# Performance work log

Measured on AMD Instinct MI355X. Metric: run time of the kernel, lower is better.

Reference implementation:

```python
import jax, jax.numpy as jnp
import numpy as np

B, S, E, H = 2, 2048, 1024, 16
D = E // H  # head_dim = 64


def setup_inputs() -> dict:
    key = jax.random.key(0)
    ks = jax.random.split(key, 6)
    scale = 1.0 / np.sqrt(E)
    x = jax.random.normal(ks[0], (B, S, E), dtype=jnp.float32)
    mask = jnp.ones((B, S), dtype=jnp.int32)
    Wqkv = jax.random.normal(ks[1], (E, 3 * E), dtype=jnp.float32) * scale
    bqkv = jax.random.normal(ks[2], (3 * E,), dtype=jnp.float32) * 0.01
    Wout = jax.random.normal(ks[3], (E, E), dtype=jnp.float32) * scale
    bout = jax.random.normal(ks[4], (E,), dtype=jnp.float32) * 0.01
    return {"x": x, "mask": mask, "Wqkv": Wqkv, "bqkv": bqkv, "Wout": Wout, "bout": bout}


def reference(x, mask, Wqkv, bqkv, Wout, bout):
    Bn, Sn, En = x.shape
    qkv = x @ Wqkv + bqkv                      # [B,S,3E]
    qkv = qkv.reshape(Bn, Sn, 3, H, D)
    qkv = jnp.transpose(qkv, (2, 0, 3, 1, 4))  # [3,B,H,S,D]
    q, k, v = qkv[0], qkv[1], qkv[2]
    scores = jnp.einsum('bhqd,bhkd->bhqk', q, k) / np.sqrt(D).astype(np.float32)
    m = mask[:, None, None, :]                 # [B,1,1,S]
    scores = jnp.where(m == 0, jnp.float32(-jnp.inf), scores)
    attn = jax.nn.softmax(scores, axis=-1)
    out = jnp.einsum('bhqk,bhkd->bhqd', attn, v)  # [B,H,S,D]
    out = jnp.transpose(out, (0, 2, 1, 3)).reshape(Bn, Sn, En)
    return out @ Wout + bout
```

## Files before the change

### kernel.cpp

```cpp
#include <hip/hip_runtime.h>


typedef __attribute__((ext_vector_type(8))) short short8;
typedef __attribute__((ext_vector_type(4))) short short4b;
typedef __attribute__((ext_vector_type(4))) float floatx4;
typedef unsigned short ushort_t;

static __device__ __forceinline__ ushort_t f2bf(float f) {
    unsigned u = __float_as_uint(f);
    u += 0x7fffu + ((u >> 16) & 1u);
    return (ushort_t)(u >> 16);
}
static __device__ __forceinline__ float bf2f(ushort_t h) {
    return __uint_as_float(((unsigned)h) << 16);
}
#if __has_builtin(__builtin_amdgcn_cvt_pk_bf16_f32)
typedef __attribute__((ext_vector_type(2))) __bf16 bf16x2_t;
static __device__ __forceinline__ unsigned pack2bf(float a, float b) {
    bf16x2_t r = __builtin_amdgcn_cvt_pk_bf16_f32(a, b);
    return __builtin_bit_cast(unsigned, r);
}
#else
static __device__ __forceinline__ unsigned pack2bf(float a, float b) {
    return (unsigned)f2bf(a) | ((unsigned)f2bf(b) << 16);
}
#endif
static __device__ __forceinline__ float hexp2(float x) {
    return __builtin_amdgcn_exp2f(x);
}
static __device__ __forceinline__ void gload16(const void* g, void* l) {
    __builtin_amdgcn_global_load_lds(
        (const __attribute__((address_space(1))) unsigned int*)g,
        (__attribute__((address_space(3))) unsigned int*)l, 16, 0, 0);
}

static __device__ __forceinline__ floatx4 mfma16(short4b a, short4b b, floatx4 c) {
#if __has_builtin(__builtin_amdgcn_mfma_f32_16x16x16_bf16)
    return __builtin_amdgcn_mfma_f32_16x16x16_bf16(a, b, c, 0, 0, 0);
#elif __has_builtin(__builtin_amdgcn_mfma_f32_16x16x16bf16_1k)
    return __builtin_amdgcn_mfma_f32_16x16x16bf16_1k(a, b, c, 0, 0, 0);
#else
    asm("v_mfma_f32_16x16x16_bf16 %0, %1, %2, %0" : "+v"(c) : "v"(a), "v"(b));
    return c;
#endif
}

__global__ __launch_bounds__(256) void prep(
    const float* __restrict__ x, ushort_t* __restrict__ xb,
    const float* __restrict__ Wqkv, ushort_t* __restrict__ wqT,
    const float* __restrict__ Wout, ushort_t* __restrict__ woT,
    const int* __restrict__ mask, float* __restrict__ maddg)
{
    __shared__ float tile[32][33];
    const int bk = blockIdx.x;
    const int t = threadIdx.x;
    if (bk < 4096) {
        int i = bk * 256 + t;
        float4 v = ((const float4*)x)[i];
        uint2 o;
        o.x = pack2bf(v.x, v.y);
        o.y = pack2bf(v.z, v.w);
        ((uint2*)xb)[i] = o;
        return;
    }
    if (bk < 8192) {
        const float* W; ushort_t* WT; int K, N, id;
        if (bk < 7168) { W = Wqkv; WT = wqT; K = 1024; N = 3072; id = bk - 4096;
                         int nb = (id % 96) * 32, kb = (id / 96) * 32;
                         const int r = t >> 3, c4 = (t & 7) * 4;
                         float4 v = *(const float4*)&W[(size_t)(kb + r) * N + nb + c4];
                         tile[r][c4+0]=v.x; tile[r][c4+1]=v.y; tile[r][c4+2]=v.z; tile[r][c4+3]=v.w;
                         __syncthreads();
                         uint2 o;
                         o.x = pack2bf(tile[c4+0][r], tile[c4+1][r]);
                         o.y = pack2bf(tile[c4+2][r], tile[c4+3][r]);
                         ((uint2*)WT)[((size_t)(nb + r) * K + kb + c4) >> 2] = o;
        } else {         W = Wout; WT = woT; K = 1024; N = 1024; id = bk - 7168;
                         int nb = (id % 32) * 32, kb = (id / 32) * 32;
                         const int r = t >> 3, c4 = (t & 7) * 4;
                         float4 v = *(const float4*)&W[(size_t)(kb + r) * N + nb + c4];
                         tile[r][c4+0]=v.x; tile[r][c4+1]=v.y; tile[r][c4+2]=v.z; tile[r][c4+3]=v.w;
                         __syncthreads();
                         uint2 o;
                         o.x = pack2bf(tile[c4+0][r], tile[c4+1][r]);
                         o.y = pack2bf(tile[c4+2][r], tile[c4+3][r]);
                         ((uint2*)WT)[((size_t)(nb + r) * K + kb + c4) >> 2] = o;
        }
        return;
    }
    {
        int i = (bk - 8192) * 256 + t;
        maddg[i] = (mask[i] ? 0.f : -1e30f) - 24.0f;
    }
}

__global__ __launch_bounds__(256, 3) void gemm_qkv(
    const ushort_t* __restrict__ A, const ushort_t* __restrict__ B,
    const float* __restrict__ bias, ushort_t* __restrict__ qkvb,
    ushort_t* __restrict__ vtg)
{
    const int K = 1024;
    __shared__ ushort_t Ah[128][32], Bh[128][32];
    __shared__ ushort_t Tb[64][136];
    const int bn = blockIdx.x * 128, bm = blockIdx.y * 128;
    const int t = threadIdx.x, w = t >> 6, lane = t & 63;
    const int l15 = lane & 15, quad = lane >> 4;
    const int wm = w >> 1, wn = w & 1;

    const int srow = w * 32 + (lane >> 2);
    const int skp  = (lane & 3) ^ ((lane >> 2) & 3);
    const int scol = skp * 8;
    const ushort_t* ga = A + (size_t)(bm + srow) * K + scol;
    const ushort_t* gb = B + (size_t)(bn + srow) * K + scol;
    const size_t rstep = (size_t)16 * K;
    const int fcol = ((quad ^ (l15 & 3)) * 8);

    floatx4 acc[4][4];
    #pragma unroll
    for (int mt = 0; mt < 4; ++mt)
        #pragma unroll
        for (int nt = 0; nt < 4; ++nt) acc[mt][nt] = (floatx4){0.f, 0.f, 0.f, 0.f};

    for (int k0 = 0; k0 < K; k0 += 32) {
        #pragma unroll
        for (int i = 0; i < 2; ++i) {
            gload16(ga + i * rstep + k0, &Ah[w * 32 + i * 16][0]);
            gload16(gb + i * rstep + k0, &Bh[w * 32 + i * 16][0]);
        }
        __syncthreads();
        short8 ah[4], bh[4];
        #pragma unroll
        for (int x = 0; x < 4; ++x) {
            ah[x] = *(const short8*)&Ah[wm * 64 + x * 16 + l15][fcol];
            bh[x] = *(const short8*)&Bh[wn * 64 + x * 16 + l15][fcol];
        }
        #pragma unroll
        for (int mt = 0; mt < 4; ++mt)
            #pragma unroll
            for (int nt = 0; nt < 4; ++nt)
                acc[mt][nt] = __builtin_amdgcn_mfma_f32_16x16x32_bf16(ah[mt], bh[nt], acc[mt][nt], 0, 0, 0);
        __syncthreads();
    }

    if (bn < 2048) {
        #pragma unroll
        for (int mt = 0; mt < 4; ++mt)
            #pragma unroll
            for (int r = 0; r < 4; ++r) {
                size_t row = (size_t)(bm + wm * 64 + mt * 16 + quad * 4 + r) * 2048;
                #pragma unroll
                for (int nt = 0; nt < 4; ++nt) {
                    int col = bn + wn * 64 + nt * 16 + l15;
                    qkvb[row + col] = f2bf(acc[mt][nt][r] + bias[col]);
                }
            }
    } else {
        const int h0 = (bn - 2048) >> 6;
        const int b  = bm >> 11, s0 = bm & 2047;
        #pragma unroll
        for (int hh = 0; hh < 2; ++hh) {
            if (wn == hh) {
                #pragma unroll
                for (int mt = 0; mt < 4; ++mt)
                    #pragma unroll
                    for (int nt = 0; nt < 4; ++nt) {
                        int d = nt * 16 + l15;
                        int sb = wm * 64 + mt * 16 + quad * 4;
                        float bv = bias[bn + hh * 64 + nt * 16 + l15];
                        uint2 pk;
                        pk.x = pack2bf(acc[mt][nt][0] + bv, acc[mt][nt][1] + bv);
                        pk.y = pack2bf(acc[mt][nt][2] + bv, acc[mt][nt][3] + bv);
                        *(uint2*)&Tb[d][sb] = pk;
                    }
            }
            __syncthreads();
            ushort_t* vbase = vtg + ((size_t)((b * 16 + h0 + hh) * 64)) * 2048 + s0;
            #pragma unroll
            for (int it = 0; it < 4; ++it) {
                int idx = t + it * 256;
                int d = idx >> 4, ch = idx & 15;
                uint4 v = *(const uint4*)&Tb[d][ch * 8];
                *(uint4*)&vbase[(size_t)d * 2048 + ch * 8] = v;
            }
            __syncthreads();
        }
    }
}

__global__ __launch_bounds__(256, 3) void gemm_bf16_f32_64(
    const ushort_t* __restrict__ A, const ushort_t* __restrict__ B,
    const float* __restrict__ bias, float* __restrict__ C,
    int M, int N, int K)
{
    __shared__ ushort_t Ah[64][32], Bh[128][32];
    const int bn = blockIdx.x * 128, bm = blockIdx.y * 64;
    const int t = threadIdx.x, w = t >> 6, lane = t & 63;
    const int l15 = lane & 15, quad = lane >> 4;
    const int wm = w >> 1, wn = w & 1;

    const int srow = w * 16 + (lane >> 2);
    const int skp  = (lane & 3) ^ ((lane >> 2) & 3);
    const int scol = skp * 8;
    const ushort_t* ga  = A + (size_t)(bm + srow) * K + scol;
    const ushort_t* gb0 = B + (size_t)(bn + srow) * K + scol;
    const ushort_t* gb1 = B + (size_t)(bn + 64 + srow) * K + scol;
    const int fcol = ((quad ^ (l15 & 3)) * 8);

    floatx4 acc[2][4];
    #pragma unroll
    for (int mt = 0; mt < 2; ++mt)
        #pragma unroll
        for (int nt = 0; nt < 4; ++nt) acc[mt][nt] = (floatx4){0.f, 0.f, 0.f, 0.f};

    for (int k0 = 0; k0 < K; k0 += 32) {
        gload16(ga  + k0, &Ah[w * 16][0]);
        gload16(gb0 + k0, &Bh[w * 16][0]);
        gload16(gb1 + k0, &Bh[64 + w * 16][0]);
        __syncthreads();
        short8 ah[2], bh[4];
        #pragma unroll
        for (int x = 0; x < 2; ++x)
            ah[x] = *(const short8*)&Ah[wm * 32 + x * 16 + l15][fcol];
        #pragma unroll
        for (int x = 0; x < 4; ++x)
            bh[x] = *(const short8*)&Bh[wn * 64 + x * 16 + l15][fcol];
        #pragma unroll
        for (int mt = 0; mt < 2; ++mt)
            #pragma unroll
            for (int nt = 0; nt < 4; ++nt)
                acc[mt][nt] = __builtin_amdgcn_mfma_f32_16x16x32_bf16(ah[mt], bh[nt], acc[mt][nt], 0, 0, 0);
        __syncthreads();
    }
    #pragma unroll
    for (int mt = 0; mt < 2; ++mt)
        #pragma unroll
        for (int r = 0; r < 4; ++r) {
            size_t row = (size_t)(bm + wm * 32 + mt * 16 + quad * 4 + r) * N;
            #pragma unroll
            for (int nt = 0; nt < 4; ++nt) {
                int col = bn + wn * 64 + nt * 16 + l15;
                C[row + col] = acc[mt][nt][r] + bias[col];
            }
        }
}

__global__ __launch_bounds__(256, 2) void flash_v7(
    const ushort_t* __restrict__ qkv, const ushort_t* __restrict__ vtg,
    const float* __restrict__ maddg, ushort_t* __restrict__ attn)
{
    __shared__ ushort_t Ks[2][64][64];
    __shared__ ushort_t Vt[2][64][64];

    const int blk = blockIdx.x;
    const int xcd = blk & 7, rr = blk >> 3;
    const int qi = rr & 15, g = xcd + 8 * (rr >> 4);
    const int b = g >> 4, h = g & 15, q0 = qi * 128;

    const int t = threadIdx.x, wave = t >> 6, lane = t & 63;
    const int l15 = lane & 15, quad = lane >> 4;
    const size_t bS = (size_t)b * 2048;
    const float c1 = 0.125f * 1.44269504088896340736f;

    short8 qf[2][2];
    #pragma unroll
    for (int tt = 0; tt < 2; ++tt) {
        int q = q0 + wave * 32 + tt * 16 + l15;
        const ushort_t* qp = qkv + (bS + q) * 2048 + h * 64;
        qf[tt][0] = *(const short8*)(qp + quad * 8);
        qf[tt][1] = *(const short8*)(qp + 32 + quad * 8);
    }

    const int srow  = wave * 16 + (lane >> 3);
    const int schnk = ((lane & 7) ^ ((lane >> 3) & 7)) * 8;
    const ushort_t* gK = qkv + (bS + srow) * 2048 + 1024 + h * 64 + schnk;
    const ushort_t* gV = vtg + ((size_t)(b * 16 + h) * 64 + srow) * 2048 + schnk;
    const float* gM = maddg + b * 2048;

    gload16(gK,            &Ks[0][wave * 16][0]);
    gload16(gK + 8 * 2048, &Ks[0][wave * 16 + 8][0]);
    gload16(gV,            &Vt[0][wave * 16][0]);
    gload16(gV + 8 * 2048, &Vt[0][wave * 16 + 8][0]);
    __syncthreads();

    floatx4 outacc[2][4];
    float lsum[2] = {0.f, 0.f};
    #pragma unroll
    for (int tt = 0; tt < 2; ++tt)
        #pragma unroll
        for (int dt = 0; dt < 4; ++dt) outacc[tt][dt] = (floatx4){0.f, 0.f, 0.f, 0.f};

    int cur = 0;
    for (int kt = 0; kt < 32; ++kt) {
        const int k0 = kt * 64;
        {
            const int kn = (kt + 1 < 32) ? (kt + 1) * 64 : 0;
            const int nb = cur ^ 1;
            gload16(gK + (size_t)kn * 2048,            &Ks[nb][wave * 16][0]);
            gload16(gK + (size_t)(kn + 8) * 2048,      &Ks[nb][wave * 16 + 8][0]);
            gload16(gV + kn,                           &Vt[nb][wave * 16][0]);
            gload16(gV + kn + 8 * 2048,                &Vt[nb][wave * 16 + 8][0]);
        }
        float4 madd4[4];
        #pragma unroll
        for (int c = 0; c < 4; ++c)
            madd4[c] = *(const float4*)&gM[k0 + c * 16 + quad * 4];

        short8 kf[2][4];
        #pragma unroll
        for (int kc = 0; kc < 2; ++kc)
            #pragma unroll
            for (int c = 0; c < 4; ++c) {
                int ch = ((kc * 4 + quad) ^ (l15 & 7)) * 8;
                kf[kc][c] = *(const short8*)&Ks[cur][c * 16 + l15][ch];
            }
        short4b vA[4][4];
        #pragma unroll
        for (int c = 0; c < 4; ++c) {
            const int vby = (((2 * c + (quad >> 1)) ^ (l15 & 7)) * 16 + (quad & 1) * 8);
            #pragma unroll
            for (int dt = 0; dt < 4; ++dt)
                vA[c][dt] = *(const short4b*)((const char*)&Vt[cur][dt * 16 + l15][0] + vby);
        }

        #pragma unroll
        for (int tt = 0; tt < 2; ++tt) {
            floatx4 sc[4];
            #pragma unroll
            for (int c = 0; c < 4; ++c) {
                sc[c] = (floatx4){0.f, 0.f, 0.f, 0.f};
                sc[c] = __builtin_amdgcn_mfma_f32_16x16x32_bf16(kf[0][c], qf[tt][0], sc[c], 0, 0, 0);
                sc[c] = __builtin_amdgcn_mfma_f32_16x16x32_bf16(kf[1][c], qf[tt][1], sc[c], 0, 0, 0);
            }
            #pragma unroll
            for (int c = 0; c < 4; ++c) {
                float p0 = hexp2(fmaf(sc[c][0], c1, madd4[c].x));
                float p1 = hexp2(fmaf(sc[c][1], c1, madd4[c].y));
                float p2 = hexp2(fmaf(sc[c][2], c1, madd4[c].z));
                float p3 = hexp2(fmaf(sc[c][3], c1, madd4[c].w));
                lsum[tt] += (p0 + p1) + (p2 + p3);
                uint2 u;
                u.x = pack2bf(p0, p1);
                u.y = pack2bf(p2, p3);
                short4b pb = __builtin_bit_cast(short4b, u);
                #pragma unroll
                for (int dt = 0; dt < 4; ++dt)
                    outacc[tt][dt] = mfma16(vA[c][dt], pb, outacc[tt][dt]);
            }
        }
        __syncthreads();
        cur ^= 1;
    }

    #pragma unroll
    for (int tt = 0; tt < 2; ++tt) {
        lsum[tt] += __shfl_xor(lsum[tt], 16);
        lsum[tt] += __shfl_xor(lsum[tt], 32);
        float inv = 1.f / lsum[tt];
        int q = q0 + wave * 32 + tt * 16 + l15;
        ushort_t* orow = attn + (bS + q) * 1024 + h * 64;
        #pragma unroll
        for (int dt = 0; dt < 4; ++dt) {
            uint2 pk;
            pk.x = pack2bf(outacc[tt][dt][0] * inv, outacc[tt][dt][1] * inv);
            pk.y = pack2bf(outacc[tt][dt][2] * inv, outacc[tt][dt][3] * inv);
            *(uint2*)&orow[dt * 16 + quad * 4] = pk;
        }
    }
}

extern "C" void kernel_launch(void* const* d_in, const int* in_sizes, int n_in,
                              void* d_out, int out_size, void* d_ws, size_t ws_size,
                              hipStream_t stream) {
    const float* x    = (const float*)d_in[0];
    const int*   mask = (const int*)  d_in[1];
    const float* Wqkv = (const float*)d_in[2];
    const float* bqkv = (const float*)d_in[3];
    const float* Wout = (const float*)d_in[4];
    const float* bout = (const float*)d_in[5];
    float* out = (float*)d_out;

    char* ws = (char*)d_ws;
    ushort_t* xb    = (ushort_t*)(ws);
    ushort_t* wqT   = (ushort_t*)(ws + 8388608);
    ushort_t* qkvb  = (ushort_t*)(ws + 14680064);
    ushort_t* vtg   = (ushort_t*)(ws + 31457280);
    ushort_t* attnb = (ushort_t*)(ws + 39845888);
    ushort_t* woT   = (ushort_t*)(ws + 48234496);
    float*    maddg = (float*)   (ws + 50331648);

    const int M = 4096, E = 1024, N3 = 3072;

    prep<<<dim3(8208), dim3(256), 0, stream>>>(
        x, xb, Wqkv, wqT, Wout, woT, mask, maddg);

    gemm_qkv<<<dim3(N3 / 128, M / 128), dim3(256), 0, stream>>>(
        xb, wqT, bqkv, qkvb, vtg);

    flash_v7<<<dim3(512), dim3(256), 0, stream>>>(qkvb, vtg, maddg, attnb);

    gemm_bf16_f32_64<<<dim3(E / 128, M / 64), dim3(256), 0, stream>>>(
        attnb, woT, bout, out, M, E, E);
}
```

Baseline: 210.4 us.

## Split flash attention block into 8 waves of 16 query rows with MFMA priority

Result: faster. 196.8 us (-6.5%).

```diff
diff --git a/kernel.cpp b/kernel.cpp
--- a/kernel.cpp
+++ b/kernel.cpp
@@ -244,7 +244,7 @@
         }
 }
 
-__global__ __launch_bounds__(256, 2) void flash_v7(
+__global__ __launch_bounds__(512, 4) void flash_v8(
     const ushort_t* __restrict__ qkv, const ushort_t* __restrict__ vtg,
     const float* __restrict__ maddg, ushort_t* __restrict__ attn)
 {
@@ -261,33 +261,28 @@
     const size_t bS = (size_t)b * 2048;
     const float c1 = 0.125f * 1.44269504088896340736f;
 
-    short8 qf[2][2];
-    #pragma unroll
-    for (int tt = 0; tt < 2; ++tt) {
-        int q = q0 + wave * 32 + tt * 16 + l15;
+    short8 qf[2];
+    {
+        int q = q0 + wave * 16 + l15;
         const ushort_t* qp = qkv + (bS + q) * 2048 + h * 64;
-        qf[tt][0] = *(const short8*)(qp + quad * 8);
-        qf[tt][1] = *(const short8*)(qp + 32 + quad * 8);
-    }
-
-    const int srow  = wave * 16 + (lane >> 3);
+        qf[0] = *(const short8*)(qp + quad * 8);
+        qf[1] = *(const short8*)(qp + 32 + quad * 8);
+    }
+
+    const int srow  = wave * 8 + (lane >> 3);
     const int schnk = ((lane & 7) ^ ((lane >> 3) & 7)) * 8;
     const ushort_t* gK = qkv + (bS + srow) * 2048 + 1024 + h * 64 + schnk;
     const ushort_t* gV = vtg + ((size_t)(b * 16 + h) * 64 + srow) * 2048 + schnk;
     const float* gM = maddg + b * 2048;
 
-    gload16(gK,            &Ks[0][wave * 16][0]);
-    gload16(gK + 8 * 2048, &Ks[0][wave * 16 + 8][0]);
-    gload16(gV,            &Vt[0][wave * 16][0]);
-    gload16(gV + 8 * 2048, &Vt[0][wave * 16 + 8][0]);
+    gload16(gK, &Ks[0][wave * 8][0]);
+    gload16(gV, &Vt[0][wave * 8][0]);
     __syncthreads();
 
-    floatx4 outacc[2][4];
-    float lsum[2] = {0.f, 0.f};
+    floatx4 outacc[4];
+    float lsum = 0.f;
     #pragma unroll
-    for (int tt = 0; tt < 2; ++tt)
-        #pragma unroll
-        for (int dt = 0; dt < 4; ++dt) outacc[tt][dt] = (floatx4){0.f, 0.f, 0.f, 0.f};
+    for (int dt = 0; dt < 4; ++dt) outacc[dt] = (floatx4){0.f, 0.f, 0.f, 0.f};
 
     int cur = 0;
     for (int kt = 0; kt < 32; ++kt) {
@@ -295,10 +290,8 @@
         {
             const int kn = (kt + 1 < 32) ? (kt + 1) * 64 : 0;
             const int nb = cur ^ 1;
-            gload16(gK + (size_t)kn * 2048,            &Ks[nb][wave * 16][0]);
-            gload16(gK + (size_t)(kn + 8) * 2048,      &Ks[nb][wave * 16 + 8][0]);
-            gload16(gV + kn,                           &Vt[nb][wave * 16][0]);
-            gload16(gV + kn + 8 * 2048,                &Vt[nb][wave * 16 + 8][0]);
+            gload16(gK + (size_t)kn * 2048, &Ks[nb][wave * 8][0]);
+            gload16(gV + kn,                &Vt[nb][wave * 8][0]);
         }
         float4 madd4[4];
         #pragma unroll
@@ -322,47 +315,47 @@
                 vA[c][dt] = *(const short4b*)((const char*)&Vt[cur][dt * 16 + l15][0] + vby);
         }
 
-        #pragma unroll
-        for (int tt = 0; tt < 2; ++tt) {
-            floatx4 sc[4];
-            #pragma unroll
-            for (int c = 0; c < 4; ++c) {
-                sc[c] = (floatx4){0.f, 0.f, 0.f, 0.f};
-                sc[c] = __builtin_amdgcn_mfma_f32_16x16x32_bf16(kf[0][c], qf[tt][0], sc[c], 0, 0, 0);
-                sc[c] = __builtin_amdgcn_mfma_f32_16x16x32_bf16(kf[1][c], qf[tt][1], sc[c], 0, 0, 0);
-            }
-            #pragma unroll
-            for (int c = 0; c < 4; ++c) {
-                float p0 = hexp2(fmaf(sc[c][0], c1, madd4[c].x));
-                float p1 = hexp2(fmaf(sc[c][1], c1, madd4[c].y));
-                float p2 = hexp2(fmaf(sc[c][2], c1, madd4[c].z));
-                float p3 = hexp2(fmaf(sc[c][3], c1, madd4[c].w));
-                lsum[tt] += (p0 + p1) + (p2 + p3);
-                uint2 u;
-                u.x = pack2bf(p0, p1);
-                u.y = pack2bf(p2, p3);
-                short4b pb = __builtin_bit_cast(short4b, u);
-                #pragma unroll
-                for (int dt = 0; dt < 4; ++dt)
-                    outacc[tt][dt] = mfma16(vA[c][dt], pb, outacc[tt][dt]);
-            }
+        floatx4 sc[4];
+        __builtin_amdgcn_s_setprio(1);
+        #pragma unroll
+        for (int c = 0; c < 4; ++c) {
+            sc[c] = (floatx4){0.f, 0.f, 0.f, 0.f};
+            sc[c] = __builtin_amdgcn_mfma_f32_16x16x32_bf16(kf[0][c], qf[0], sc[c], 0, 0, 0);
+            sc[c] = __builtin_amdgcn_mfma_f32_16x16x32_bf16(kf[1][c], qf[1], sc[c], 0, 0, 0);
+        }
+        __builtin_amdgcn_s_setprio(0);
+        #pragma unroll
+        for (int c = 0; c < 4; ++c) {
+            float p0 = hexp2(fmaf(sc[c][0], c1, madd4[c].x));
+            float p1 = hexp2(fmaf(sc[c][1], c1, madd4[c].y));
+            float p2 = hexp2(fmaf(sc[c][2], c1, madd4[c].z));
+            float p3 = hexp2(fmaf(sc[c][3], c1, madd4[c].w));
+            lsum += (p0 + p1) + (p2 + p3);
+            uint2 u;
+            u.x = pack2bf(p0, p1);
+            u.y = pack2bf(p2, p3);
+            short4b pb = __builtin_bit_cast(short4b, u);
+            __builtin_amdgcn_s_setprio(1);
+            #pragma unroll
+            for (int dt = 0; dt < 4; ++dt)
+                outacc[dt] = mfma16(vA[c][dt], pb, outacc[dt]);
+            __builtin_amdgcn_s_setprio(0);
         }
         __syncthreads();
         cur ^= 1;
     }
 
-    #pragma unroll
-    for (int tt = 0; tt < 2; ++tt) {
-        lsum[tt] += __shfl_xor(lsum[tt], 16);
-        lsum[tt] += __shfl_xor(lsum[tt], 32);
-        float inv = 1.f / lsum[tt];
-        int q = q0 + wave * 32 + tt * 16 + l15;
+    {
+        lsum += __shfl_xor(lsum, 16);
+        lsum += __shfl_xor(lsum, 32);
+        float inv = 1.f / lsum;
+        int q = q0 + wave * 16 + l15;
         ushort_t* orow = attn + (bS + q) * 1024 + h * 64;
         #pragma unroll
         for (int dt = 0; dt < 4; ++dt) {
             uint2 pk;
-            pk.x = pack2bf(outacc[tt][dt][0] * inv, outacc[tt][dt][1] * inv);
-            pk.y = pack2bf(outacc[tt][dt][2] * inv, outacc[tt][dt][3] * inv);
+            pk.x = pack2bf(outacc[dt][0] * inv, outacc[dt][1] * inv);
+            pk.y = pack2bf(outacc[dt][2] * inv, outacc[dt][3] * inv);
             *(uint2*)&orow[dt * 16 + quad * 4] = pk;
         }
     }
@@ -396,7 +389,7 @@
     gemm_qkv<<<dim3(N3 / 128, M / 128), dim3(256), 0, stream>>>(
         xb, wqT, bqkv, qkvb, vtg);
 
-    flash_v7<<<dim3(512), dim3(256), 0, stream>>>(qkvb, vtg, maddg, attnb);
+    flash_v8<<<dim3(512), dim3(512), 0, stream>>>(qkvb, vtg, maddg, attnb);
 
     gemm_bf16_f32_64<<<dim3(E / 128, M / 64), dim3(256), 0, stream>>>(
         attnb, woT, bout, out, M, E, E);
```
